# Optimization experiments

Measured on AMD Instinct MI355X. Metric: run time of the kernel, lower is better.

## Reference

```python
import jax, jax.numpy as jnp
import numpy as np

OWN_DIM = 7
INTR_DIM = 5
N_HEADS = 3
HEAD_DIM = 5
N_INTR = 256
BATCH = 32768
H1, H2 = 256, 256
ACTION_DIM = 2
IN_DIM = OWN_DIM + N_HEADS * HEAD_DIM  # 22
SCALE = np.sqrt(HEAD_DIM).astype(np.float32)
LN_EPS = 1e-5


def setup_inputs() -> dict:
    key = jax.random.key(0)
    ks = jax.random.split(key, 16)
    f32 = jnp.float32
    inp = {
        "obs": jax.random.normal(ks[0], (BATCH, OWN_DIM + N_INTR * INTR_DIM), dtype=f32),
        "Wq": jax.random.normal(ks[1], (N_HEADS, OWN_DIM, HEAD_DIM), dtype=f32) * 0.4,
        "bq": jnp.zeros((N_HEADS, HEAD_DIM), dtype=f32),
        "Wk": jax.random.normal(ks[2], (N_HEADS, INTR_DIM, HEAD_DIM), dtype=f32) * 0.4,
        "bk": jnp.zeros((N_HEADS, HEAD_DIM), dtype=f32),
        "Wv": jax.random.normal(ks[3], (N_HEADS, INTR_DIM, HEAD_DIM), dtype=f32) * 0.4,
        "bv": jnp.zeros((N_HEADS, HEAD_DIM), dtype=f32),
        "v_att": jax.random.normal(ks[4], (N_HEADS, HEAD_DIM), dtype=f32) * 0.5,
        "temperature": jnp.ones((1,), dtype=f32) * 3.0,
        "ln_g": jnp.ones((IN_DIM,), dtype=f32),
        "ln_b": jnp.zeros((IN_DIM,), dtype=f32),
        "W1": jax.random.normal(ks[5], (IN_DIM, H1), dtype=f32) * 0.15,
        "b1": jnp.zeros((H1,), dtype=f32),
        "W2": jax.random.normal(ks[6], (H1, H2), dtype=f32) * 0.08,
        "b2": jnp.zeros((H2,), dtype=f32),
        "Wf": jax.random.normal(ks[7], (H2, ACTION_DIM), dtype=f32) * 0.08,
        "bf": jnp.zeros((ACTION_DIM,), dtype=f32),
        "log_std": jnp.zeros((ACTION_DIM,), dtype=f32),
    }
    return inp


def reference(obs, Wq, bq, Wk, bk, Wv, bv, v_att, temperature,
              ln_g, ln_b, W1, b1, W2, b2, Wf, bf, log_std):
    own = obs[:, :OWN_DIM]                                   # [B, 7]
    intr = obs[:, OWN_DIM:OWN_DIM + N_INTR * INTR_DIM]
    intr = intr.reshape(-1, N_INTR, INTR_DIM)                # [B, N, 5]

    # all heads at once
    q = jnp.einsum("bo,hod->bhd", own, Wq) + bq              # [B, H, D]
    k = jnp.einsum("bni,hid->bhnd", intr, Wk) + bk[None, :, None, :]
    v = jnp.einsum("bni,hid->bhnd", intr, Wv) + bv[None, :, None, :]

    energy = jnp.tanh(q[:, :, None, :] + k)                  # [B, H, N, D]
    scores = jnp.einsum("bhnd,hd->bhn", energy, v_att)
    scores = scores / SCALE * jnp.abs(temperature[0])

    is_padding = jnp.sum(jnp.abs(intr), axis=2) < 1e-6       # [B, N]
    scores = jnp.where(is_padding[:, None, :], -jnp.inf, scores)
    alpha = jax.nn.softmax(scores, axis=-1)
    alpha = jnp.nan_to_num(alpha, nan=0.0)                   # all-padded rows -> 0

    context = jnp.einsum("bhn,bhnd->bhd", alpha, v)          # [B, H, D]
    context = context.reshape(context.shape[0], N_HEADS * HEAD_DIM)

    x = jnp.concatenate([own, context], axis=1)              # [B, 22]
    mu = jnp.mean(x, axis=-1, keepdims=True)
    var = jnp.mean(jnp.square(x - mu), axis=-1, keepdims=True)
    x = (x - mu) * jax.lax.rsqrt(var + LN_EPS) * ln_g + ln_b

    x = jax.nn.leaky_relu(x @ W1 + b1, negative_slope=0.2)
    x = jax.nn.leaky_relu(x @ W2 + b2, negative_slope=0.2)
    out = x @ Wf + bf                                        # [B, 2]

    log_std_exp = jnp.broadcast_to(log_std[None, :], (out.shape[0], ACTION_DIM))
    return jnp.concatenate([out, log_std_exp], axis=1)       # [B, 4]
```

## Files before the change

kernel.cpp:

```cpp
#include <hip/hip_runtime.h>
#include <math.h>

#define NBATCH   32768
#define OWN_DIM  7
#define INTR_DIM 5
#define N_HEADS  3
#define HEAD_DIM 5
#define N_INTR   256
#define ROWLEN   1287
#define XDIM     22
#define H1DIM    256
#define H2DIM    256

typedef __attribute__((ext_vector_type(8))) short bf16x8;
typedef __attribute__((ext_vector_type(4))) float f32x4;

__device__ __forceinline__ float fast_tanh(float x) {
    float e = __builtin_amdgcn_exp2f(x * 2.885390081777927f);
    return 1.0f - 2.0f * __builtin_amdgcn_rcpf(e + 1.0f);
}

__device__ __forceinline__ float leaky02(float x) {
    return fmaxf(x, 0.2f * x);
}

__device__ __forceinline__ unsigned short f2bf_rne(float f) {
    unsigned u = __float_as_uint(f);
    return (unsigned short)((u + 0x7FFFu + ((u >> 16) & 1u)) >> 16);
}

__global__ __launch_bounds__(256, 2) void attn_ln_kernel(
    const float* __restrict__ obs,
    const float* __restrict__ Wq, const float* __restrict__ bq,
    const float* __restrict__ Wk, const float* __restrict__ bk,
    const float* __restrict__ Wv, const float* __restrict__ bv,
    const float* __restrict__ v_att, const float* __restrict__ temp,
    const float* __restrict__ ln_g, const float* __restrict__ ln_b,
    float* __restrict__ xout)
{
    const int wid  = threadIdx.x >> 6;
    const int lane = threadIdx.x & 63;
    const int s    = blockIdx.x * 4 + wid;
    const float* row = obs + (size_t)s * ROWLEN;

    const float fac = fabsf(temp[0]) * 0.4472135954999579f;
    const float facl2e = fac * 1.4426950408889634f;

    float own[OWN_DIM];
    #pragma unroll
    for (int o = 0; o < OWN_DIM; ++o) own[o] = row[o];

    float xi[4][INTR_DIM];
    float npf[4];
    #pragma unroll
    for (int r = 0; r < 4; ++r) {
        const float* it = row + OWN_DIM + (lane + 64*r) * INTR_DIM;
        #pragma unroll
        for (int i = 0; i < INTR_DIM; ++i) xi[r][i] = it[i];
        float asum = fabsf(xi[r][0]) + fabsf(xi[r][1]) + fabsf(xi[r][2])
                   + fabsf(xi[r][3]) + fabsf(xi[r][4]);
        npf[r] = (asum < 1e-6f) ? 0.0f : 1.0f;
    }

    float svp[N_HEADS][INTR_DIM];
    float es[N_HEADS];

    #pragma unroll
    for (int h = 0; h < N_HEADS; ++h) {
        float wk[INTR_DIM][HEAD_DIM];
        #pragma unroll
        for (int i = 0; i < INTR_DIM; ++i)
            #pragma unroll
            for (int d = 0; d < HEAD_DIM; ++d)
                wk[i][d] = Wk[h*INTR_DIM*HEAD_DIM + i*HEAD_DIM + d];
        float va[HEAD_DIM];
        #pragma unroll
        for (int d = 0; d < HEAD_DIM; ++d)
            va[d] = v_att[h*HEAD_DIM + d] * facl2e;
        float qb[HEAD_DIM];
        #pragma unroll
        for (int d = 0; d < HEAD_DIM; ++d) {
            float a = bq[h*HEAD_DIM + d] + bk[h*HEAD_DIM + d];
            #pragma unroll
            for (int o = 0; o < OWN_DIM; ++o)
                a = fmaf(own[o], Wq[h*OWN_DIM*HEAD_DIM + o*HEAD_DIM + d], a);
            qb[d] = a;
        }

        float sv0 = 0.f, sv1 = 0.f, sv2 = 0.f, sv3 = 0.f, sv4 = 0.f, esum = 0.f;
        #pragma unroll
        for (int r = 0; r < 4; ++r) {
            float dot = 0.0f;
            #pragma unroll
            for (int d = 0; d < HEAD_DIM; ++d) {
                float t = qb[d];
                #pragma unroll
                for (int i = 0; i < INTR_DIM; ++i)
                    t = fmaf(xi[r][i], wk[i][d], t);
                dot = fmaf(fast_tanh(t), va[d], dot);
            }
            float e = npf[r] * __builtin_amdgcn_exp2f(dot);
            esum += e;
            sv0 = fmaf(e, xi[r][0], sv0);
            sv1 = fmaf(e, xi[r][1], sv1);
            sv2 = fmaf(e, xi[r][2], sv2);
            sv3 = fmaf(e, xi[r][3], sv3);
            sv4 = fmaf(e, xi[r][4], sv4);
        }
        svp[h][0] = sv0; svp[h][1] = sv1; svp[h][2] = sv2;
        svp[h][3] = sv3; svp[h][4] = sv4; es[h] = esum;
    }

    #pragma unroll
    for (int o = 1; o < 64; o <<= 1) {
        #pragma unroll
        for (int h = 0; h < N_HEADS; ++h) {
            es[h] += __shfl_xor(es[h], o, 64);
            #pragma unroll
            for (int i = 0; i < INTR_DIM; ++i)
                svp[h][i] += __shfl_xor(svp[h][i], o, 64);
        }
    }

    float ctx[N_HEADS][HEAD_DIM];
    #pragma unroll
    for (int h = 0; h < N_HEADS; ++h) {
        const float live = (es[h] > 0.0f) ? 1.0f : 0.0f;
        const float rinv = live * __builtin_amdgcn_rcpf(es[h]);
        float svn[INTR_DIM];
        #pragma unroll
        for (int i = 0; i < INTR_DIM; ++i) svn[i] = svp[h][i] * rinv;
        #pragma unroll
        for (int d = 0; d < HEAD_DIM; ++d) {
            float c = bv[h*HEAD_DIM + d] * live;
            #pragma unroll
            for (int i = 0; i < INTR_DIM; ++i)
                c = fmaf(svn[i], Wv[h*INTR_DIM*HEAD_DIM + i*HEAD_DIM + d], c);
            ctx[h][d] = c;
        }
    }

    float sum = 0.0f;
    #pragma unroll
    for (int o = 0; o < OWN_DIM; ++o) sum += own[o];
    #pragma unroll
    for (int h = 0; h < N_HEADS; ++h)
        #pragma unroll
        for (int d = 0; d < HEAD_DIM; ++d) sum += ctx[h][d];
    const float mu = sum * (1.0f / 22.0f);
    float var = 0.0f;
    #pragma unroll
    for (int o = 0; o < OWN_DIM; ++o) { float dd = own[o] - mu; var += dd*dd; }
    #pragma unroll
    for (int h = 0; h < N_HEADS; ++h)
        #pragma unroll
        for (int d = 0; d < HEAD_DIM; ++d) { float dd = ctx[h][d] - mu; var += dd*dd; }
    var *= (1.0f / 22.0f);
    const float rs = rsqrtf(var + 1e-5f);

    float xv = own[0];
    #pragma unroll
    for (int o = 1; o < OWN_DIM; ++o) xv = (lane == o) ? own[o] : xv;
    #pragma unroll
    for (int j = 0; j < 15; ++j) xv = (lane == OWN_DIM + j) ? ctx[j/5][j%5] : xv;
    if (lane < XDIM) {
        xout[(size_t)s * XDIM + lane] = (xv - mu) * rs * ln_g[lane] + ln_b[lane];
    }
}

__global__ __launch_bounds__(256) void mlp_kernel(
    const float* __restrict__ x,
    const float* __restrict__ W1, const float* __restrict__ b1,
    const float* __restrict__ W2, const float* __restrict__ b2,
    const float* __restrict__ Wf, const float* __restrict__ bf,
    const float* __restrict__ lstd, float* __restrict__ out)
{
    __shared__ __align__(16) float xs[32 * XDIM];
    __shared__ __align__(16) unsigned char h1b[32 * 256 * 2];
    __shared__ __align__(16) unsigned char w2b[256 * 64 * 2];
    __shared__ __align__(16) float wfs[H2DIM * 2];
    __shared__ float oacc[4][32][2];

    const int t   = threadIdx.x;
    const int blk = blockIdx.x;

    for (int i = t; i < 32 * XDIM; i += 256) xs[i] = x[(size_t)blk * 32 * XDIM + i];
    for (int i = t; i < H2DIM * 2; i += 256) wfs[i] = Wf[i];

    float w1r[XDIM];
    #pragma unroll
    for (int i = 0; i < XDIM; ++i) w1r[i] = W1[i * H1DIM + t];
    const float b1t = b1[t];
    __syncthreads();
    for (int e = 0; e < 32; ++e) {
        float a = b1t;
        #pragma unroll
        for (int i = 0; i < XDIM; ++i) a += xs[e * XDIM + i] * w1r[i];
        a = leaky02(a);
        int byte = e * 512 + t * 2;
        byte ^= ((e & 7) << 4);
        *(unsigned short*)(h1b + byte) = f2bf_rne(a);
    }

    const int wv_  = t >> 6;
    const int lane = t & 63;
    const int mrow = lane & 15;
    const int qk   = lane >> 4;

    f32x4 acc[2][4];
    #pragma unroll
    for (int mt = 0; mt < 2; ++mt)
        #pragma unroll
        for (int nt = 0; nt < 4; ++nt)
            acc[mt][nt] = (f32x4){0.f, 0.f, 0.f, 0.f};

    for (int kc = 0; kc < 4; ++kc) {
        __syncthreads();
        {
            const int n = t;
            #pragma unroll
            for (int k8 = 0; k8 < 64; k8 += 8) {
                bf16x8 v;
                #pragma unroll
                for (int j = 0; j < 8; ++j) {
                    float w = W2[(size_t)(kc * 64 + k8 + j) * H2DIM + n];
                    v[j] = (short)f2bf_rne(w);
                }
                int byte = n * 128 + k8 * 2;
                byte ^= ((n & 7) << 4);
                *(bf16x8*)(w2b + byte) = v;
            }
        }
        __syncthreads();
        #pragma unroll
        for (int ks = 0; ks < 2; ++ks) {
            const int klocal = ks * 32;
            const int kglob  = kc * 64 + klocal;
            bf16x8 afrag[2], bfrag[4];
            #pragma unroll
            for (int mt = 0; mt < 2; ++mt) {
                const int rowi = mt * 16 + mrow;
                int byte = rowi * 512 + (kglob + 8 * qk) * 2;
                byte ^= ((rowi & 7) << 4);
                afrag[mt] = *(const bf16x8*)(h1b + byte);
            }
            #pragma unroll
            for (int nt = 0; nt < 4; ++nt) {
                const int col = wv_ * 64 + nt * 16 + mrow;
                int byte = col * 128 + (klocal + 8 * qk) * 2;
                byte ^= ((col & 7) << 4);
                bfrag[nt] = *(const bf16x8*)(w2b + byte);
            }
            #pragma unroll
            for (int mt = 0; mt < 2; ++mt)
                #pragma unroll
                for (int nt = 0; nt < 4; ++nt)
                    acc[mt][nt] = __builtin_amdgcn_mfma_f32_16x16x32_bf16(
                        afrag[mt], bfrag[nt], acc[mt][nt], 0, 0, 0);
        }
    }

    float b2n[4];
    #pragma unroll
    for (int nt = 0; nt < 4; ++nt) b2n[nt] = b2[wv_ * 64 + nt * 16 + mrow];

    float p[8][2];
    #pragma unroll
    for (int i = 0; i < 8; ++i) { p[i][0] = 0.f; p[i][1] = 0.f; }
    #pragma unroll
    for (int mt = 0; mt < 2; ++mt)
        #pragma unroll
        for (int nt = 0; nt < 4; ++nt) {
            const int n = wv_ * 64 + nt * 16 + mrow;
            #pragma unroll
            for (int reg = 0; reg < 4; ++reg) {
                float h2v = leaky02(acc[mt][nt][reg] + b2n[nt]);
                p[mt*4 + reg][0] = fmaf(h2v, wfs[2*n + 0], p[mt*4 + reg][0]);
                p[mt*4 + reg][1] = fmaf(h2v, wfs[2*n + 1], p[mt*4 + reg][1]);
            }
        }
    #pragma unroll
    for (int o = 1; o < 16; o <<= 1) {
        #pragma unroll
        for (int i = 0; i < 8; ++i) {
            p[i][0] += __shfl_xor(p[i][0], o, 64);
            p[i][1] += __shfl_xor(p[i][1], o, 64);
        }
    }
    if (mrow == 0) {
        #pragma unroll
        for (int mt = 0; mt < 2; ++mt)
            #pragma unroll
            for (int reg = 0; reg < 4; ++reg) {
                const int sample = mt * 16 + qk * 4 + reg;
                oacc[wv_][sample][0] = p[mt*4 + reg][0];
                oacc[wv_][sample][1] = p[mt*4 + reg][1];
            }
    }
    __syncthreads();
    if (t < 32) {
        float o0 = bf[0], o1 = bf[1];
        #pragma unroll
        for (int w = 0; w < 4; ++w) { o0 += oacc[w][t][0]; o1 += oacc[w][t][1]; }
        float4 o4;
        o4.x = o0; o4.y = o1; o4.z = lstd[0]; o4.w = lstd[1];
        *(float4*)&out[(size_t)(blk * 32 + t) * 4] = o4;
    }
}

extern "C" void kernel_launch(void* const* d_in, const int* in_sizes, int n_in,
                              void* d_out, int out_size, void* d_ws, size_t ws_size,
                              hipStream_t stream) {
    const float* obs   = (const float*)d_in[0];
    const float* Wq    = (const float*)d_in[1];
    const float* bq    = (const float*)d_in[2];
    const float* Wk    = (const float*)d_in[3];
    const float* bk    = (const float*)d_in[4];
    const float* Wv    = (const float*)d_in[5];
    const float* bv    = (const float*)d_in[6];
    const float* v_att = (const float*)d_in[7];
    const float* temp  = (const float*)d_in[8];
    const float* ln_g  = (const float*)d_in[9];
    const float* ln_b  = (const float*)d_in[10];
    const float* W1    = (const float*)d_in[11];
    const float* b1    = (const float*)d_in[12];
    const float* W2    = (const float*)d_in[13];
    const float* b2    = (const float*)d_in[14];
    const float* Wf    = (const float*)d_in[15];
    const float* bf    = (const float*)d_in[16];
    const float* lstd  = (const float*)d_in[17];

    float* xbuf = (float*)d_ws;
    float* outf = (float*)d_out;

    attn_ln_kernel<<<NBATCH / 4, 256, 0, stream>>>(
        obs, Wq, bq, Wk, bk, Wv, bv, v_att, temp, ln_g, ln_b, xbuf);
    mlp_kernel<<<NBATCH / 32, 256, 0, stream>>>(
        xbuf, W1, b1, W2, b2, Wf, bf, lstd, outf);
}
```

Measured before the change: 107.5 us.

## Map four samples per wavefront and fold tanh constants into score dot

Each wavefront now processes four batch rows with 16 lanes apiece instead of one row per 64 lanes. Each lane loops over 16 intruders, with all three heads computed per loaded intruder. The cross-lane reduction shrinks from six to four shuffle stages, and the tanh's 1 - 2*rcp form is folded algebraically into a precomputed v_att sum plus scaled weights. The aim is to cut shuffle and reduction overhead and redundant per-head work. The cost is more per-lane registers and a strided load pattern within each 16-lane group.

```diff
diff --git a/kernel.cpp b/kernel.cpp
--- a/kernel.cpp
+++ b/kernel.cpp
@@ -14,11 +14,6 @@
 
 typedef __attribute__((ext_vector_type(8))) short bf16x8;
 typedef __attribute__((ext_vector_type(4))) float f32x4;
-
-__device__ __forceinline__ float fast_tanh(float x) {
-    float e = __builtin_amdgcn_exp2f(x * 2.885390081777927f);
-    return 1.0f - 2.0f * __builtin_amdgcn_rcpf(e + 1.0f);
-}
 
 __device__ __forceinline__ float leaky02(float x) {
     return fmaxf(x, 0.2f * x);
@@ -40,79 +35,79 @@
 {
     const int wid  = threadIdx.x >> 6;
     const int lane = threadIdx.x & 63;
-    const int s    = blockIdx.x * 4 + wid;
+    const int grp  = lane >> 4;
+    const int gl   = lane & 15;
+    const int s    = blockIdx.x * 16 + wid * 4 + grp;
     const float* row = obs + (size_t)s * ROWLEN;
 
     const float fac = fabsf(temp[0]) * 0.4472135954999579f;
     const float facl2e = fac * 1.4426950408889634f;
+    const float TL2E = 2.885390081777927f;
 
     float own[OWN_DIM];
     #pragma unroll
     for (int o = 0; o < OWN_DIM; ++o) own[o] = row[o];
 
-    float xi[4][INTR_DIM];
-    float npf[4];
-    #pragma unroll
-    for (int r = 0; r < 4; ++r) {
-        const float* it = row + OWN_DIM + (lane + 64*r) * INTR_DIM;
-        #pragma unroll
-        for (int i = 0; i < INTR_DIM; ++i) xi[r][i] = it[i];
-        float asum = fabsf(xi[r][0]) + fabsf(xi[r][1]) + fabsf(xi[r][2])
-                   + fabsf(xi[r][3]) + fabsf(xi[r][4]);
-        npf[r] = (asum < 1e-6f) ? 0.0f : 1.0f;
-    }
-
-    float svp[N_HEADS][INTR_DIM];
-    float es[N_HEADS];
-
+    float va2[N_HEADS][HEAD_DIM], vasum[N_HEADS];
     #pragma unroll
     for (int h = 0; h < N_HEADS; ++h) {
-        float wk[INTR_DIM][HEAD_DIM];
-        #pragma unroll
-        for (int i = 0; i < INTR_DIM; ++i)
-            #pragma unroll
-            for (int d = 0; d < HEAD_DIM; ++d)
-                wk[i][d] = Wk[h*INTR_DIM*HEAD_DIM + i*HEAD_DIM + d];
-        float va[HEAD_DIM];
-        #pragma unroll
-        for (int d = 0; d < HEAD_DIM; ++d)
-            va[d] = v_att[h*HEAD_DIM + d] * facl2e;
-        float qb[HEAD_DIM];
+        float ssum = 0.0f;
+        #pragma unroll
+        for (int d = 0; d < HEAD_DIM; ++d) {
+            float v = v_att[h*HEAD_DIM + d];
+            ssum += v;
+            va2[h][d] = v * (-2.0f * facl2e);
+        }
+        vasum[h] = ssum * facl2e;
+    }
+
+    float qb[N_HEADS][HEAD_DIM];
+    #pragma unroll
+    for (int h = 0; h < N_HEADS; ++h)
         #pragma unroll
         for (int d = 0; d < HEAD_DIM; ++d) {
             float a = bq[h*HEAD_DIM + d] + bk[h*HEAD_DIM + d];
             #pragma unroll
             for (int o = 0; o < OWN_DIM; ++o)
                 a = fmaf(own[o], Wq[h*OWN_DIM*HEAD_DIM + o*HEAD_DIM + d], a);
-            qb[d] = a;
-        }
-
-        float sv0 = 0.f, sv1 = 0.f, sv2 = 0.f, sv3 = 0.f, sv4 = 0.f, esum = 0.f;
-        #pragma unroll
-        for (int r = 0; r < 4; ++r) {
-            float dot = 0.0f;
+            qb[h][d] = a;
+        }
+
+    float svp[N_HEADS][INTR_DIM] = {};
+    float es[N_HEADS] = {};
+
+    #pragma unroll
+    for (int r = 0; r < 16; ++r) {
+        const float* it = row + OWN_DIM + (gl + 16*r) * INTR_DIM;
+        float xi[INTR_DIM];
+        #pragma unroll
+        for (int i = 0; i < INTR_DIM; ++i) xi[i] = it[i];
+        float asum = fabsf(xi[0]) + fabsf(xi[1]) + fabsf(xi[2])
+                   + fabsf(xi[3]) + fabsf(xi[4]);
+        const float npf = (asum < 1e-6f) ? 0.0f : 1.0f;
+        #pragma unroll
+        for (int h = 0; h < N_HEADS; ++h) {
+            float dot = vasum[h];
             #pragma unroll
             for (int d = 0; d < HEAD_DIM; ++d) {
-                float t = qb[d];
+                float t = qb[h][d];
                 #pragma unroll
                 for (int i = 0; i < INTR_DIM; ++i)
-                    t = fmaf(xi[r][i], wk[i][d], t);
-                dot = fmaf(fast_tanh(t), va[d], dot);
-            }
-            float e = npf[r] * __builtin_amdgcn_exp2f(dot);
-            esum += e;
-            sv0 = fmaf(e, xi[r][0], sv0);
-            sv1 = fmaf(e, xi[r][1], sv1);
-            sv2 = fmaf(e, xi[r][2], sv2);
-            sv3 = fmaf(e, xi[r][3], sv3);
-            sv4 = fmaf(e, xi[r][4], sv4);
-        }
-        svp[h][0] = sv0; svp[h][1] = sv1; svp[h][2] = sv2;
-        svp[h][3] = sv3; svp[h][4] = sv4; es[h] = esum;
-    }
-
-    #pragma unroll
-    for (int o = 1; o < 64; o <<= 1) {
+                    t = fmaf(xi[i], Wk[h*INTR_DIM*HEAD_DIM + i*HEAD_DIM + d], t);
+                float e = __builtin_amdgcn_exp2f(t * TL2E);
+                float rc = __builtin_amdgcn_rcpf(e + 1.0f);
+                dot = fmaf(va2[h][d], rc, dot);
+            }
+            float e = npf * __builtin_amdgcn_exp2f(dot);
+            es[h] += e;
+            #pragma unroll
+            for (int i = 0; i < INTR_DIM; ++i)
+                svp[h][i] = fmaf(e, xi[i], svp[h][i]);
+        }
+    }
+
+    #pragma unroll
+    for (int o = 1; o < 16; o <<= 1) {
         #pragma unroll
         for (int h = 0; h < N_HEADS; ++h) {
             es[h] += __shfl_xor(es[h], o, 64);
@@ -158,13 +153,19 @@
     var *= (1.0f / 22.0f);
     const float rs = rsqrtf(var + 1e-5f);
 
-    float xv = own[0];
-    #pragma unroll
-    for (int o = 1; o < OWN_DIM; ++o) xv = (lane == o) ? own[o] : xv;
-    #pragma unroll
-    for (int j = 0; j < 15; ++j) xv = (lane == OWN_DIM + j) ? ctx[j/5][j%5] : xv;
-    if (lane < XDIM) {
-        xout[(size_t)s * XDIM + lane] = (xv - mu) * rs * ln_g[lane] + ln_b[lane];
+    float xv0 = own[0];
+    #pragma unroll
+    for (int o = 1; o < OWN_DIM; ++o) xv0 = (gl == o) ? own[o] : xv0;
+    #pragma unroll
+    for (int j = 0; j < 15; ++j) xv0 = (gl == OWN_DIM + j) ? ctx[j/5][j%5] : xv0;
+    float xv1 = ctx[1][4];
+    #pragma unroll
+    for (int j = 10; j < 15; ++j) xv1 = (gl == j - 9) ? ctx[j/5][j%5] : xv1;
+
+    float* xo = xout + (size_t)s * XDIM;
+    xo[gl] = (xv0 - mu) * rs * ln_g[gl] + ln_b[gl];
+    if (gl < XDIM - 16) {
+        xo[16 + gl] = (xv1 - mu) * rs * ln_g[16 + gl] + ln_b[16 + gl];
     }
 }
 
@@ -333,7 +334,7 @@
     float* xbuf = (float*)d_ws;
     float* outf = (float*)d_out;
 
-    attn_ln_kernel<<<NBATCH / 4, 256, 0, stream>>>(
+    attn_ln_kernel<<<NBATCH / 16, 256, 0, stream>>>(
         obs, Wq, bq, Wk, bk, Wv, bv, v_att, temp, ln_g, ln_b, xbuf);
     mlp_kernel<<<NBATCH / 32, 256, 0, stream>>>(
         xbuf, W1, b1, W2, b2, Wf, bf, lstd, outf);
```

Result: faster. 91.36 us (-15.0%).
